# Kernel optimization log

Measured on AMD Instinct MI355X. Metric: run time of the kernel, lower is better.

Reference implementation:

```python
import jax, jax.numpy as jnp
import numpy as np


def _tanh_approx(x):
    return x * jax.lax.rsqrt(1.0 + x * x)


def _lru(u, nu_log, gamma_log, Bm, Cm, Dv):
    # u: [B,T,H]; nu_log/gamma_log: [N]; Bm: [N,H]; Cm: [H,N]; Dv: [H]
    A = jnp.exp(-jnp.exp(nu_log))                       # [N], |A|<1
    Bu = jnp.exp(gamma_log) * jnp.einsum('bth,nh->btn', u, Bm)  # [B,T,N]
    A_full = jnp.broadcast_to(A, Bu.shape)
    # diagonal linear recurrence h_t = A*h_{t-1} + Bu_t via parallel scan
    def comb(c1, c2):
        a1, b1 = c1
        a2, b2 = c2
        return (a1 * a2, a2 * b1 + b2)
    _, h = jax.lax.associative_scan(comb, (A_full, Bu), axis=1)  # inclusive scan
    # module uses the state delayed by one step (out[0]=0, out[t]=h_{t-1})
    h_prev = jnp.pad(h[:, :-1, :], ((0, 0), (1, 0), (0, 0)))
    y = jnp.einsum('btn,hn->bth', h_prev, Cm) + Dv * u
    return y


def _model_block(x, nu_log, gamma_log, Bm, Cm, Dv, Wlin, blin):
    y = _lru(x, nu_log, gamma_log, Bm, Cm, Dv)
    y = _tanh_approx(y) @ Wlin.T + blin
    return y + x


def setup_inputs() -> dict:
    key = jax.random.key(0)
    ks = jax.random.split(key, 10)
    B_, T_, N, H, D = 16, 65536, 64, 64, 4
    r_min, r_max = 0.8, 1.0
    u = jax.random.uniform(ks[0], (D, N))
    nu_log = jnp.log(-0.5 * jnp.log(u * (r_max ** 2 - r_min ** 2) + r_min ** 2))
    A = jnp.exp(-jnp.exp(nu_log))
    gamma_log = jnp.log(jnp.sqrt(1.0 - A ** 2))
    Bm = jax.random.normal(ks[1], (D, N, H)) / np.sqrt(2.0 * H)
    Cm = jax.random.normal(ks[2], (D, H, N)) / np.sqrt(N)
    Dv = jax.random.normal(ks[3], (D, H))
    Wlin = jax.random.normal(ks[4], (D, H, H)) / np.sqrt(H)
    blin = jnp.zeros((D, H))
    Win = jax.random.normal(ks[5], (H, 1))
    Wout = jax.random.normal(ks[6], (1, H)) / np.sqrt(H)
    x = jax.random.normal(ks[7], (B_, T_, 1))
    return {"x": x, "Win": Win, "nu_log": nu_log, "gamma_log": gamma_log,
            "Bm": Bm, "Cm": Cm, "Dv": Dv, "Wlin": Wlin, "blin": blin, "Wout": Wout}


def reference(x, Win, nu_log, gamma_log, Bm, Cm, Dv, Wlin, blin, Wout):
    h = x @ Win.T  # [B,T,H]
    depth = nu_log.shape[0]
    for i in range(depth):
        h = _model_block(h, nu_log[i], gamma_log[i], Bm[i], Cm[i], Dv[i], Wlin[i], blin[i])
    return h @ Wout.T  # [B,T,1]
```

## Files before the change

### kernel.cpp

```cpp
#include <hip/hip_runtime.h>

#define B_ 16
#define T_ 65536
#define H_ 64
#define DEPTH_ 4
#define CHUNK 128
#define NCH (T_ / CHUNK)

typedef _Float16 f16;
typedef f16 f16x8 __attribute__((ext_vector_type(8)));
typedef float f32x4 __attribute__((ext_vector_type(4)));
typedef unsigned u32x4 __attribute__((ext_vector_type(4)));

#define MFMA(a, b, c) __builtin_amdgcn_mfma_f32_16x16x32_f16(a, b, c, 0, 0, 0)
#define SWZ(t, k) ((t) * 64 + ((k) ^ (((t) & 7) << 2)))

union U4F8 { u32x4 u; f16x8 h; };

__device__ __forceinline__ f16x8 ldfrag(const f16* p) { return *(const f16x8*)p; }

__global__ __launch_bounds__(256)
void prep(const float* __restrict__ Win, const float* __restrict__ nu,
          const float* __restrict__ ga, const float* __restrict__ Bm,
          const float* __restrict__ Cm, const float* __restrict__ Dv,
          const float* __restrict__ Wl,
          f16* __restrict__ BmH, f16* __restrict__ BmL,
          f16* __restrict__ CmH, f16* __restrict__ CmL,
          f16* __restrict__ WlH, float* __restrict__ atab, float* __restrict__ sc)
{
    const int tid = threadIdx.x;
    for (int l = 0; l < DEPTH_; ++l) {
        for (int idx = tid; idx < 4096; idx += 256) {
            int n = idx >> 6;
            float g = expf(ga[l * 64 + n]);
            float v = Bm[l * 4096 + idx] * g;
            f16 h = (f16)v;
            BmH[l * 4096 + idx] = h;
            BmL[l * 4096 + idx] = (f16)(v - (float)h);
            float cv = Cm[l * 4096 + idx];
            h = (f16)cv;
            CmH[l * 4096 + idx] = h;
            CmL[l * 4096 + idx] = (f16)(cv - (float)h);
            WlH[l * 4096 + idx] = (f16)Wl[l * 4096 + idx];
        }
        if (tid < 64) {
            int n = tid;
            float ex = expf(nu[l * 64 + n]);
            float a = expf(-ex);
            float g = expf(ga[l * 64 + n]);
            sc[l * 320 + n] = a;
            sc[l * 320 + 64 + n] = Dv[l * 64 + n];
            float bw = 0.f;
            for (int h2 = 0; h2 < 64; ++h2) bw += Bm[l * 4096 + n * 64 + h2] * Win[h2];
            sc[l * 320 + 128 + n] = bw * g;
            sc[l * 320 + 192 + n] = Dv[l * 64 + n] * Win[n];
            sc[l * 320 + 256 + n] = Win[n];
        }
        for (int idx = tid; idx < 8192; idx += 256) {
            int n = idx >> 7, j = idx & 127;
            float ex = expf(nu[l * 64 + n]);
            atab[l * 8192 + idx] = expf(-ex * (float)j);
        }
    }
}

__global__ __launch_bounds__(64)
void carry_x(const float* __restrict__ x, const float* __restrict__ sc0,
             float* __restrict__ carry)
{
    const int blk = blockIdx.x;
    const int b = blk >> 9, c = blk & (NCH - 1);
    const int n = threadIdx.x;
    const float a  = sc0[n];
    const float bw = sc0[128 + n];
    __shared__ float xs[64];
    const float* xp = x + (size_t)b * T_ + c * CHUNK;
    float s = 0.f;
    for (int bb = 0; bb < CHUNK / 64; ++bb) {
        __syncthreads();
        xs[n] = xp[bb * 64 + n];
        __syncthreads();
        #pragma unroll
        for (int tt = 0; tt < 64; ++tt) s = a * s + bw * xs[tt];
    }
    carry[((size_t)b * NCH + c) * 64 + n] = s;
}

__global__ __launch_bounds__(256)
void scan_carry(const float* __restrict__ nu_log, float* __restrict__ carry)
{
    const int b = blockIdx.x;
    const int tid = threadIdx.x;
    const int n = tid & 63, q = tid >> 6;
    const float ex = expf(nu_log[n]);
    const float aL = expf(-ex * (float)CHUNK);
    float* cp = carry + (size_t)b * NCH * 64 + n;
    __shared__ float part[4][64];

    const int SEG = NCH / 4;
    const int base = q * SEG;
    float p = 0.f;
    #pragma unroll 4
    for (int i = 0; i < SEG; ++i) {
        float v = cp[(size_t)(base + i) * 64];
        cp[(size_t)(base + i) * 64] = p;
        p = aL * p + v;
    }
    part[q][n] = p;
    __syncthreads();
    if (q > 0) {
        const float aLS = expf(-ex * (float)(CHUNK * SEG));
        float inc = 0.f;
        for (int qq = 0; qq < q; ++qq) inc = inc * aLS + part[qq][n];
        float qv = inc;
        #pragma unroll 4
        for (int i = 0; i < SEG; ++i) {
            cp[(size_t)(base + i) * 64] += qv;
            qv *= aL;
        }
    }
}

struct LPrep {
    const f16 *BmH, *BmL, *CmH, *CmL, *WlH;
    const float *av, *dvv, *bw, *dwin, *win;
    const f16 *BmHn, *BmLn;
    const float *atabn;
    const float *blin, *Wout;
};

template<int IN_X, int OUT_FINAL>
__global__ __launch_bounds__(256, 4)
void lru_fused(const float* __restrict__ x, f16* __restrict__ ubuf,
               LPrep P, float* __restrict__ carry, float* __restrict__ out)
{
    const int blk = blockIdx.x;
    const int b = blk >> 9, c = blk & (NCH - 1);
    const int t0 = c * CHUNK;
    const int tid = threadIdx.x;
    const int w = tid >> 6, lane = tid & 63;
    const int l15 = lane & 15, lq = lane >> 4;

    __shared__ float hpk[CHUNK * 64];
    __shared__ float swv[4][64];
    __shared__ float red[4][64];

    f16* ug = ubuf + ((size_t)b * T_ + t0) * 64;
    const float* xg = x + (size_t)b * T_ + t0;

    f16x8 ahu[2][2];
    if (!IN_X) {
        #pragma unroll
        for (int tt = 0; tt < 2; ++tt) {
            const f16* p = ug + (size_t)((2 * w + tt) * 16 + l15) * 64;
            U4F8 r0, r1;
            r0.u = __builtin_nontemporal_load((const u32x4*)(p + lq * 8));
            r1.u = __builtin_nontemporal_load((const u32x4*)(p + 32 + lq * 8));
            ahu[tt][0] = r0.h;
            ahu[tt][1] = r1.h;
        }
    }

    float av4[4];
    #pragma unroll
    for (int nt = 0; nt < 4; ++nt) av4[nt] = P.av[nt * 16 + l15];

    float xv[2][4];
    if (IN_X) {
        #pragma unroll
        for (int tt = 0; tt < 2; ++tt)
            #pragma unroll
            for (int r = 0; r < 4; ++r)
                xv[tt][r] = xg[32 * w + 16 * tt + 4 * lq + r];
    }

    f32x4 acc[4][2];
    if (IN_X) {
        #pragma unroll
        for (int nt = 0; nt < 4; ++nt) {
            float bwn = P.bw[nt * 16 + l15];
            #pragma unroll
            for (int tt = 0; tt < 2; ++tt)
                #pragma unroll
                for (int r = 0; r < 4; ++r) acc[nt][tt][r] = xv[tt][r] * bwn;
        }
    } else {
        #pragma unroll
        for (int nt = 0; nt < 4; ++nt) {
            int n = nt * 16 + l15;
            f16x8 bh0 = ldfrag(P.BmH + n * 64 + lq * 8);
            f16x8 bh1 = ldfrag(P.BmH + n * 64 + 32 + lq * 8);
            f16x8 bl0 = ldfrag(P.BmL + n * 64 + lq * 8);
            f16x8 bl1 = ldfrag(P.BmL + n * 64 + 32 + lq * 8);
            #pragma unroll
            for (int tt = 0; tt < 2; ++tt) {
                f32x4 a4v = {0.f, 0.f, 0.f, 0.f};
                a4v = MFMA(ahu[tt][0], bh0, a4v);
                a4v = MFMA(ahu[tt][0], bl0, a4v);
                a4v = MFMA(ahu[tt][1], bh1, a4v);
                a4v = MFMA(ahu[tt][1], bl1, a4v);
                acc[nt][tt] = a4v;
            }
        }
    }

    float Wb[4][2];
    #pragma unroll
    for (int nt = 0; nt < 4; ++nt) {
        float a = av4[nt], a2 = a * a, a4 = a2 * a2, a8 = a4 * a4, a16 = a8 * a8;
        float P0incl = 0.f;
        #pragma unroll
        for (int tt = 0; tt < 2; ++tt) {
            f32x4 xs = acc[nt][tt];
            float L0 = xs[0];
            float L1 = a * L0 + xs[1];
            float L2 = a * L1 + xs[2];
            float Cv = a * L2 + xs[3];
            float u1 = __shfl_up(Cv, 16);
            float t1 = Cv + ((lq >= 1) ? a4 * u1 : 0.f);
            float u2 = __shfl_up(t1, 32);
            float Pv = t1 + ((lq >= 2) ? a8 * u2 : 0.f);
            float E = __shfl_up(Pv, 16);
            E = (lq == 0) ? 0.f : E;
            if (tt == 0) { Wb[nt][0] = E; P0incl = Pv; }
            else {
                float B0 = __shfl(P0incl, 48 + l15);
                float a4lq = 1.f;
                if (lq & 1) a4lq *= a4;
                if (lq & 2) a4lq *= a8;
                Wb[nt][1] = E + a4lq * B0;
                if (lq == 3) swv[w][nt * 16 + l15] = Pv + a16 * B0;
            }
        }
    }
    __syncthreads();

    #pragma unroll
    for (int nt = 0; nt < 4; ++nt) {
        int n = nt * 16 + l15;
        float a = av4[nt], a2 = a * a, a4 = a2 * a2, a8 = a4 * a4, a16 = a8 * a8, a32 = a16 * a16;
        float inc = carry[((size_t)b * NCH + c) * 64 + n];
        for (int ww = 0; ww < w; ++ww) inc = inc * a32 + swv[ww][n];
        float a4lq = 1.f;
        if (lq & 1) a4lq *= a4;
        if (lq & 2) a4lq *= a8;
        #pragma unroll
        for (int tt = 0; tt < 2; ++tt) {
            float Z = Wb[nt][tt] + a4lq * (tt ? a16 : 1.f) * inc;
            float s = Z;
            #pragma unroll
            for (int r = 0; r < 4; ++r) {
                int t = 32 * w + 16 * tt + 4 * lq + r;
                hpk[SWZ(t, n)] = s;
                s = a * s + acc[nt][tt][r];
            }
        }
    }

    #pragma unroll
    for (int tt = 0; tt < 2; ++tt) {
        int tb = 2 * w + tt, trow = tb * 16 + l15, sw = (trow & 7) << 2;
        const float* hw = hpk + trow * 64;
        f16x8 ah[2], al[2];
        #pragma unroll
        for (int kk = 0; kk < 2; ++kk) {
            int kb = kk * 32 + lq * 8;
            float4 v0 = *(const float4*)(hw + (kb ^ sw));
            float4 v1 = *(const float4*)(hw + ((kb + 4) ^ sw));
            float vv[8] = {v0.x, v0.y, v0.z, v0.w, v1.x, v1.y, v1.z, v1.w};
            #pragma unroll
            for (int i = 0; i < 8; ++i) {
                f16 h = (f16)vv[i];
                ah[kk][i] = h;
                al[kk][i] = (f16)(vv[i] - (float)h);
            }
        }
        #pragma unroll
        for (int nt = 0; nt < 4; ++nt) {
            int n = nt * 16 + l15;
            f16x8 ch0 = ldfrag(P.CmH + n * 64 + lq * 8);
            f16x8 ch1 = ldfrag(P.CmH + n * 64 + 32 + lq * 8);
            f16x8 cl0 = ldfrag(P.CmL + n * 64 + lq * 8);
            f16x8 cl1 = ldfrag(P.CmL + n * 64 + 32 + lq * 8);
            f32x4 a4v = {0.f, 0.f, 0.f, 0.f};
            a4v = MFMA(ah[0], ch0, a4v);
            a4v = MFMA(al[0], ch0, a4v);
            a4v = MFMA(ah[0], cl0, a4v);
            a4v = MFMA(ah[1], ch1, a4v);
            a4v = MFMA(al[1], ch1, a4v);
            a4v = MFMA(ah[1], cl1, a4v);
            if (!IN_X) {
                float dv = P.dvv[n];
                f16 dh = (f16)dv, dl = (f16)(dv - (float)dh);
                f16x8 dfh, dfl;
                #pragma unroll
                for (int i2 = 0; i2 < 8; ++i2) { dfh[i2] = (f16)0.f; dfl[i2] = (f16)0.f; }
                int e = ((nt & 1) * 16 + l15) - lq * 8;
                if (e >= 0 && e < 8) { dfh[e] = dh; dfl[e] = dl; }
                a4v = MFMA(ahu[tt][nt >> 1], dfh, a4v);
                a4v = MFMA(ahu[tt][nt >> 1], dfl, a4v);
            }
            float dwin = IN_X ? P.dwin[n] : 0.f;
            #pragma unroll
            for (int r = 0; r < 4; ++r) {
                int t = tb * 16 + lq * 4 + r;
                float y = a4v[r];
                if (IN_X) y += xv[tt][r] * dwin;
                hpk[SWZ(t, n)] = y * rsqrtf(1.f + y * y);
            }
        }
    }

    f16* stg = (f16*)hpk;
    #pragma unroll
    for (int tt = 0; tt < 2; ++tt) {
        int tb = 2 * w + tt, trow = tb * 16 + l15, sw = (trow & 7) << 2;
        const float* hw = hpk + trow * 64;
        f16x8 t0f, t1f;
        #pragma unroll
        for (int kk = 0; kk < 2; ++kk) {
            int kb = kk * 32 + lq * 8;
            float4 v0 = *(const float4*)(hw + (kb ^ sw));
            float4 v1 = *(const float4*)(hw + ((kb + 4) ^ sw));
            float vv[8] = {v0.x, v0.y, v0.z, v0.w, v1.x, v1.y, v1.z, v1.w};
            #pragma unroll
            for (int i = 0; i < 8; ++i) {
                if (kk == 0) t0f[i] = (f16)vv[i]; else t1f[i] = (f16)vv[i];
            }
        }
        float val[4] = {0.f, 0.f, 0.f, 0.f};
        #pragma unroll
        for (int nt = 0; nt < 4; ++nt) {
            int n = nt * 16 + l15;
            f16x8 w0f = ldfrag(P.WlH + n * 64 + lq * 8);
            f16x8 w1f = ldfrag(P.WlH + n * 64 + 32 + lq * 8);
            f32x4 a4v = {0.f, 0.f, 0.f, 0.f};
            a4v = MFMA(t0f, w0f, a4v);
            a4v = MFMA(t1f, w1f, a4v);
            if (!IN_X) {
                f16x8 ifr;
                #pragma unroll
                for (int i2 = 0; i2 < 8; ++i2) ifr[i2] = (f16)0.f;
                int e = ((nt & 1) * 16 + l15) - lq * 8;
                if (e >= 0 && e < 8) ifr[e] = (f16)1.f;
                a4v = MFMA(ahu[tt][nt >> 1], ifr, a4v);
            }
            float blj = P.blin[n];
            float wij = IN_X ? P.win[n] : 0.f;
            float woj = OUT_FINAL ? P.Wout[n] : 0.f;
            #pragma unroll
            for (int r = 0; r < 4; ++r) {
                int t = tb * 16 + lq * 4 + r;
                float o = a4v[r] + blj;
                if (IN_X) o += xv[tt][r] * wij;
                if (OUT_FINAL) {
                    val[r] += o * woj;
                } else {
                    int g = n >> 1;
                    int word = t * 64 + (((g & ~3) ^ ((t & 7) << 2)) | (g & 3));
                    stg[word * 2 + (n & 1)] = (f16)o;
                }
            }
        }
        if (OUT_FINAL) {
            #pragma unroll
            for (int r = 0; r < 4; ++r) {
                float p = val[r];
                p += __shfl_xor(p, 1);
                p += __shfl_xor(p, 2);
                p += __shfl_xor(p, 4);
                p += __shfl_xor(p, 8);
                if (l15 == 0) out[(size_t)b * T_ + t0 + tb * 16 + lq * 4 + r] = p;
            }
        }
    }

    if (!OUT_FINAL) {
        #pragma unroll
        for (int i = 0; i < 4; ++i) {
            int row = 32 * w + i * 8 + (lane >> 3);
            int gg = 4 * (lane & 7);
            int word = row * 64 + (gg ^ ((row & 7) << 2));
            u32x4 cv = *(const u32x4*)(hpk + word);
            __builtin_nontemporal_store(cv, (u32x4*)(ug + (size_t)row * 64 + 8 * (lane & 7)));
        }

        float partial[4] = {0.f, 0.f, 0.f, 0.f};
        #pragma unroll
        for (int tt = 0; tt < 2; ++tt) {
            int tb = 2 * w + tt, arow = tb * 16 + l15, msk = (arow & 7) << 2;
            U4F8 av0, av1;
            av0.u = *(const u32x4*)(hpk + arow * 64 + ((4 * lq) ^ msk));
            av1.u = *(const u32x4*)(hpk + arow * 64 + ((16 + 4 * lq) ^ msk));
            #pragma unroll
            for (int nt = 0; nt < 4; ++nt) {
                int n = nt * 16 + l15;
                f16x8 bh0 = ldfrag(P.BmHn + n * 64 + lq * 8);
                f16x8 bh1 = ldfrag(P.BmHn + n * 64 + 32 + lq * 8);
                f16x8 bl0 = ldfrag(P.BmLn + n * 64 + lq * 8);
                f16x8 bl1 = ldfrag(P.BmLn + n * 64 + 32 + lq * 8);
                f32x4 a4v = {0.f, 0.f, 0.f, 0.f};
                a4v = MFMA(av0.h, bh0, a4v);
                a4v = MFMA(av0.h, bl0, a4v);
                a4v = MFMA(av1.h, bh1, a4v);
                a4v = MFMA(av1.h, bl1, a4v);
                float4 dp = *(const float4*)(P.atabn + n * 128 + 124 - tb * 16 - lq * 4);
                partial[nt] += a4v[0] * dp.w + a4v[1] * dp.z + a4v[2] * dp.y + a4v[3] * dp.x;
            }
        }
        #pragma unroll
        for (int nt = 0; nt < 4; ++nt) {
            float v = partial[nt];
            v += __shfl_xor(v, 16);
            v += __shfl_xor(v, 32);
            if (lq == 0) red[w][nt * 16 + l15] = v;
        }
        __syncthreads();
        if (w == 0)
            carry[((size_t)b * NCH + c) * 64 + lane] =
                red[0][lane] + red[1][lane] + red[2][lane] + red[3][lane];
    }
}

extern "C" void kernel_launch(void* const* d_in, const int* in_sizes, int n_in,
                              void* d_out, int out_size, void* d_ws, size_t ws_size,
                              hipStream_t stream)
{
    const float* x   = (const float*)d_in[0];
    const float* Win = (const float*)d_in[1];
    const float* nu  = (const float*)d_in[2];
    const float* ga  = (const float*)d_in[3];
    const float* Bm  = (const float*)d_in[4];
    const float* Cm  = (const float*)d_in[5];
    const float* Dv  = (const float*)d_in[6];
    const float* Wl  = (const float*)d_in[7];
    const float* bl  = (const float*)d_in[8];
    const float* Wo  = (const float*)d_in[9];
    float* out = (float*)d_out;

    char* p = (char*)d_ws;
    f16* ubuf = (f16*)p;            p += (size_t)B_ * T_ * 64 * sizeof(f16);
    float* carry = (float*)p;       p += (size_t)B_ * NCH * 64 * sizeof(float);
    f16* wBmH = (f16*)p;            p += 4 * 4096 * sizeof(f16);
    f16* wBmL = (f16*)p;            p += 4 * 4096 * sizeof(f16);
    f16* wCmH = (f16*)p;            p += 4 * 4096 * sizeof(f16);
    f16* wCmL = (f16*)p;            p += 4 * 4096 * sizeof(f16);
    f16* wWlH = (f16*)p;            p += 4 * 4096 * sizeof(f16);
    float* atab = (float*)p;        p += 4 * 8192 * sizeof(float);
    float* sc = (float*)p;          p += 4 * 320 * sizeof(float);

    dim3 grid(B_ * NCH), blk256(256), blk64(64), gscan(B_);

    prep<<<1, 256, 0, stream>>>(Win, nu, ga, Bm, Cm, Dv, Wl,
                                wBmH, wBmL, wCmH, wCmL, wWlH, atab, sc);
    carry_x<<<grid, blk64, 0, stream>>>(x, sc, carry);

    for (int l = 0; l < DEPTH_; ++l) {
        int ln = (l + 1 < DEPTH_) ? l + 1 : l;
        scan_carry<<<gscan, blk256, 0, stream>>>(nu + l * 64, carry);
        LPrep Pr;
        Pr.BmH = wBmH + l * 4096;  Pr.BmL = wBmL + l * 4096;
        Pr.CmH = wCmH + l * 4096;  Pr.CmL = wCmL + l * 4096;
        Pr.WlH = wWlH + l * 4096;
        Pr.av = sc + l * 320;       Pr.dvv = sc + l * 320 + 64;
        Pr.bw = sc + l * 320 + 128; Pr.dwin = sc + l * 320 + 192;
        Pr.win = sc + l * 320 + 256;
        Pr.BmHn = wBmH + ln * 4096; Pr.BmLn = wBmL + ln * 4096;
        Pr.atabn = atab + ln * 8192;
        Pr.blin = bl + l * 64; Pr.Wout = Wo;
        if (l == 0)
            lru_fused<1, 0><<<grid, blk256, 0, stream>>>(x, ubuf, Pr, carry, out);
        else if (l == DEPTH_ - 1)
            lru_fused<0, 1><<<grid, blk256, 0, stream>>>(x, ubuf, Pr, carry, out);
        else
            lru_fused<0, 0><<<grid, blk256, 0, stream>>>(x, ubuf, Pr, carry, out);
    }
}
```

Before: 1.410 ms.

## Precompute diagonal MFMA fragments, pack f16 conversions, and raise MFMA wave priority

```diff
diff --git a/kernel.cpp b/kernel.cpp
--- a/kernel.cpp
+++ b/kernel.cpp
@@ -9,15 +9,40 @@
 
 typedef _Float16 f16;
 typedef f16 f16x8 __attribute__((ext_vector_type(8)));
+typedef __fp16 fp16x2 __attribute__((ext_vector_type(2)));
 typedef float f32x4 __attribute__((ext_vector_type(4)));
 typedef unsigned u32x4 __attribute__((ext_vector_type(4)));
 
 #define MFMA(a, b, c) __builtin_amdgcn_mfma_f32_16x16x32_f16(a, b, c, 0, 0, 0)
 #define SWZ(t, k) ((t) * 64 + ((k) ^ (((t) & 7) << 2)))
+#define SP1() __builtin_amdgcn_s_setprio(1)
+#define SP0() __builtin_amdgcn_s_setprio(0)
 
 union U4F8 { u32x4 u; f16x8 h; };
 
 __device__ __forceinline__ f16x8 ldfrag(const f16* p) { return *(const f16x8*)p; }
+
+__device__ __forceinline__ void split8(const float* vv, f16x8* hi, f16x8* lo)
+{
+    union { f16x8 v; fp16x2 p[4]; } H, L;
+    #pragma unroll
+    for (int i = 0; i < 4; ++i) {
+        fp16x2 h = __builtin_amdgcn_cvt_pkrtz(vv[2 * i], vv[2 * i + 1]);
+        H.p[i] = h;
+        L.p[i] = __builtin_amdgcn_cvt_pkrtz(vv[2 * i] - (float)h[0],
+                                            vv[2 * i + 1] - (float)h[1]);
+    }
+    *hi = H.v; *lo = L.v;
+}
+
+__device__ __forceinline__ f16x8 pack8(const float* vv)
+{
+    union { f16x8 v; fp16x2 p[4]; } H;
+    #pragma unroll
+    for (int i = 0; i < 4; ++i)
+        H.p[i] = __builtin_amdgcn_cvt_pkrtz(vv[2 * i], vv[2 * i + 1]);
+    return H.v;
+}
 
 __global__ __launch_bounds__(256)
 void prep(const float* __restrict__ Win, const float* __restrict__ nu,
@@ -26,7 +51,8 @@
           const float* __restrict__ Wl,
           f16* __restrict__ BmH, f16* __restrict__ BmL,
           f16* __restrict__ CmH, f16* __restrict__ CmL,
-          f16* __restrict__ WlH, float* __restrict__ atab, float* __restrict__ sc)
+          f16* __restrict__ WlH, float* __restrict__ atab, float* __restrict__ sc,
+          f16* __restrict__ tdh, f16* __restrict__ tdl, f16* __restrict__ tid1)
 {
     const int tid = threadIdx.x;
     for (int l = 0; l < DEPTH_; ++l) {
@@ -61,6 +87,17 @@
             float ex = expf(nu[l * 64 + n]);
             atab[l * 8192 + idx] = expf(-ex * (float)j);
         }
+        for (int idx = tid; idx < 2048; idx += 256) {
+            int nt = idx >> 9, lane = (idx >> 3) & 63, i = idx & 7;
+            int l15v = lane & 15, lqv = lane >> 4;
+            int e = ((nt & 1) * 16 + l15v) - lqv * 8;
+            float dv = Dv[l * 64 + nt * 16 + l15v];
+            f16 dh = (f16)dv;
+            f16 dl = (f16)(dv - (float)dh);
+            tdh[l * 2048 + idx] = (i == e) ? dh : (f16)0.f;
+            tdl[l * 2048 + idx] = (i == e) ? dl : (f16)0.f;
+            if (l == 0) tid1[idx] = (i == e) ? (f16)1.f : (f16)0.f;
+        }
     }
 }
 
@@ -127,6 +164,7 @@
     const f16 *BmHn, *BmLn;
     const float *atabn;
     const float *blin, *Wout;
+    const f16 *tdh, *tdl, *tid1;
 };
 
 template<int IN_X, int OUT_FINAL>
@@ -192,6 +230,7 @@
             f16x8 bh1 = ldfrag(P.BmH + n * 64 + 32 + lq * 8);
             f16x8 bl0 = ldfrag(P.BmL + n * 64 + lq * 8);
             f16x8 bl1 = ldfrag(P.BmL + n * 64 + 32 + lq * 8);
+            SP1();
             #pragma unroll
             for (int tt = 0; tt < 2; ++tt) {
                 f32x4 a4v = {0.f, 0.f, 0.f, 0.f};
@@ -201,6 +240,7 @@
                 a4v = MFMA(ahu[tt][1], bl1, a4v);
                 acc[nt][tt] = a4v;
             }
+            SP0();
         }
     }
 
@@ -268,12 +308,7 @@
             float4 v0 = *(const float4*)(hw + (kb ^ sw));
             float4 v1 = *(const float4*)(hw + ((kb + 4) ^ sw));
             float vv[8] = {v0.x, v0.y, v0.z, v0.w, v1.x, v1.y, v1.z, v1.w};
-            #pragma unroll
-            for (int i = 0; i < 8; ++i) {
-                f16 h = (f16)vv[i];
-                ah[kk][i] = h;
-                al[kk][i] = (f16)(vv[i] - (float)h);
-            }
+            split8(vv, &ah[kk], &al[kk]);
         }
         #pragma unroll
         for (int nt = 0; nt < 4; ++nt) {
@@ -282,7 +317,13 @@
             f16x8 ch1 = ldfrag(P.CmH + n * 64 + 32 + lq * 8);
             f16x8 cl0 = ldfrag(P.CmL + n * 64 + lq * 8);
             f16x8 cl1 = ldfrag(P.CmL + n * 64 + 32 + lq * 8);
+            f16x8 dfh, dfl;
+            if (!IN_X) {
+                dfh = ldfrag(P.tdh + ((nt * 64 + lane) << 3));
+                dfl = ldfrag(P.tdl + ((nt * 64 + lane) << 3));
+            }
             f32x4 a4v = {0.f, 0.f, 0.f, 0.f};
+            SP1();
             a4v = MFMA(ah[0], ch0, a4v);
             a4v = MFMA(al[0], ch0, a4v);
             a4v = MFMA(ah[0], cl0, a4v);
@@ -290,16 +331,10 @@
             a4v = MFMA(al[1], ch1, a4v);
             a4v = MFMA(ah[1], cl1, a4v);
             if (!IN_X) {
-                float dv = P.dvv[n];
-                f16 dh = (f16)dv, dl = (f16)(dv - (float)dh);
-                f16x8 dfh, dfl;
-                #pragma unroll
-                for (int i2 = 0; i2 < 8; ++i2) { dfh[i2] = (f16)0.f; dfl[i2] = (f16)0.f; }
-                int e = ((nt & 1) * 16 + l15) - lq * 8;
-                if (e >= 0 && e < 8) { dfh[e] = dh; dfl[e] = dl; }
                 a4v = MFMA(ahu[tt][nt >> 1], dfh, a4v);
                 a4v = MFMA(ahu[tt][nt >> 1], dfl, a4v);
             }
+            SP0();
             float dwin = IN_X ? P.dwin[n] : 0.f;
             #pragma unroll
             for (int r = 0; r < 4; ++r) {
@@ -323,10 +358,7 @@
             float4 v0 = *(const float4*)(hw + (kb ^ sw));
             float4 v1 = *(const float4*)(hw + ((kb + 4) ^ sw));
             float vv[8] = {v0.x, v0.y, v0.z, v0.w, v1.x, v1.y, v1.z, v1.w};
-            #pragma unroll
-            for (int i = 0; i < 8; ++i) {
-                if (kk == 0) t0f[i] = (f16)vv[i]; else t1f[i] = (f16)vv[i];
-            }
+            if (kk == 0) t0f = pack8(vv); else t1f = pack8(vv);
         }
         float val[4] = {0.f, 0.f, 0.f, 0.f};
         #pragma unroll
@@ -334,17 +366,14 @@
             int n = nt * 16 + l15;
             f16x8 w0f = ldfrag(P.WlH + n * 64 + lq * 8);
             f16x8 w1f = ldfrag(P.WlH + n * 64 + 32 + lq * 8);
+            f16x8 ifr;
+            if (!IN_X) ifr = ldfrag(P.tid1 + ((nt * 64 + lane) << 3));
             f32x4 a4v = {0.f, 0.f, 0.f, 0.f};
+            SP1();
             a4v = MFMA(t0f, w0f, a4v);
             a4v = MFMA(t1f, w1f, a4v);
-            if (!IN_X) {
-                f16x8 ifr;
-                #pragma unroll
-                for (int i2 = 0; i2 < 8; ++i2) ifr[i2] = (f16)0.f;
-                int e = ((nt & 1) * 16 + l15) - lq * 8;
-                if (e >= 0 && e < 8) ifr[e] = (f16)1.f;
-                a4v = MFMA(ahu[tt][nt >> 1], ifr, a4v);
-            }
+            if (!IN_X) a4v = MFMA(ahu[tt][nt >> 1], ifr, a4v);
+            SP0();
             float blj = P.blin[n];
             float wij = IN_X ? P.win[n] : 0.f;
             float woj = OUT_FINAL ? P.Wout[n] : 0.f;
@@ -400,10 +429,12 @@
                 f16x8 bl0 = ldfrag(P.BmLn + n * 64 + lq * 8);
                 f16x8 bl1 = ldfrag(P.BmLn + n * 64 + 32 + lq * 8);
                 f32x4 a4v = {0.f, 0.f, 0.f, 0.f};
+                SP1();
                 a4v = MFMA(av0.h, bh0, a4v);
                 a4v = MFMA(av0.h, bl0, a4v);
                 a4v = MFMA(av1.h, bh1, a4v);
                 a4v = MFMA(av1.h, bl1, a4v);
+                SP0();
                 float4 dp = *(const float4*)(P.atabn + n * 128 + 124 - tb * 16 - lq * 4);
                 partial[nt] += a4v[0] * dp.w + a4v[1] * dp.z + a4v[2] * dp.y + a4v[3] * dp.x;
             }
@@ -448,11 +479,15 @@
     f16* wWlH = (f16*)p;            p += 4 * 4096 * sizeof(f16);
     float* atab = (float*)p;        p += 4 * 8192 * sizeof(float);
     float* sc = (float*)p;          p += 4 * 320 * sizeof(float);
+    f16* tdh = (f16*)p;             p += 4 * 2048 * sizeof(f16);
+    f16* tdl = (f16*)p;             p += 4 * 2048 * sizeof(f16);
+    f16* tid1 = (f16*)p;            p += 2048 * sizeof(f16);
 
     dim3 grid(B_ * NCH), blk256(256), blk64(64), gscan(B_);
 
     prep<<<1, 256, 0, stream>>>(Win, nu, ga, Bm, Cm, Dv, Wl,
-                                wBmH, wBmL, wCmH, wCmL, wWlH, atab, sc);
+                                wBmH, wBmL, wCmH, wCmL, wWlH, atab, sc,
+                                tdh, tdl, tid1);
     carry_x<<<grid, blk64, 0, stream>>>(x, sc, carry);
 
     for (int l = 0; l < DEPTH_; ++l) {
@@ -468,6 +503,7 @@
         Pr.BmHn = wBmH + ln * 4096; Pr.BmLn = wBmL + ln * 4096;
         Pr.atabn = atab + ln * 8192;
         Pr.blin = bl + l * 64; Pr.Wout = Wo;
+        Pr.tdh = tdh + l * 2048; Pr.tdl = tdl + l * 2048; Pr.tid1 = tid1;
         if (l == 0)
             lru_fused<1, 0><<<grid, blk256, 0, stream>>>(x, ubuf, Pr, carry, out);
         else if (l == DEPTH_ - 1)
```

Result: slower. 1.640 ms (+16.3%).
